# Kernel optimization log

Hardware: AMD Instinct MI355X
Metric: run time of the kernel (lower is better)

## Reference

```python
import jax, jax.numpy as jnp
import numpy as np

D_MODEL = 1024
D_STATE = 16
BATCH = 2
SEQ = 2048


def setup_inputs() -> dict:
    key = jax.random.key(0)
    k1, k2, k3, k4, k5 = jax.random.split(key, 5)
    x = jax.random.normal(k1, (BATCH, SEQ, D_MODEL), dtype=jnp.float32)
    log_A_diag = jax.random.normal(k2, (D_MODEL, D_STATE), dtype=jnp.float32)
    B_w = jax.random.normal(k3, (D_STATE, D_MODEL), dtype=jnp.float32) / np.sqrt(D_MODEL)
    C_w = jax.random.normal(k4, (D_MODEL, D_STATE), dtype=jnp.float32) / np.sqrt(D_STATE)
    D_vec = jax.random.normal(k5, (D_MODEL,), dtype=jnp.float32)
    return {"x": x, "log_A_diag": log_A_diag, "B_w": B_w, "C_w": C_w, "D_vec": D_vec}


def reference(x, log_A_diag, B_w, C_w, D_vec):
    # x: (B, L, D)
    B, L, D = x.shape
    pad = 2 * L
    A_bar = jnp.exp(-jnp.exp(log_A_diag))          # (D, S), in (0, 1)
    B_t = jnp.einsum('bld,sd->bls', x, B_w)        # B projection: (B, L, S)
    k_idx = jnp.arange(L, dtype=x.dtype)
    kernel = A_bar[..., None] ** k_idx             # (D, S, L) exponential kernel
    # zero-padded FFT convolution along time axis
    kernel_fft = jnp.fft.rfft(kernel, n=pad, axis=-1)                 # (D, S, L+1)
    B_fft = jnp.fft.rfft(B_t.transpose(0, 2, 1), n=pad, axis=-1)      # (B, S, L+1)
    conv_fft = kernel_fft[None] * B_fft[:, None]                      # (B, D, S, L+1)
    conv = jnp.fft.irfft(conv_fft, n=pad, axis=-1)[..., :L]           # (B, D, S, L)
    # C projection fused over state dim; equivalent to permute->einsum('blds,ds->bld')
    y = jnp.einsum('bdsl,ds->bld', conv, C_w)
    y = y + D_vec[None, None, :] * x               # skip connection
    return y  # dropout is identity in eval mode
```

## Files before the change

### kernel.cpp

```cpp
#include <hip/hip_runtime.h>

#define D_MODEL 1024
#define D_STATE 16
#define BATCH   2
#define SEQ     2048
#define CHUNK   32
#define NCHUNK  (SEQ / CHUNK)
#define NGRP    (SEQ / 4)

__global__ __launch_bounds__(256) void k_bt(const float* __restrict__ x,
                                            const float* __restrict__ Bw,
                                            float* __restrict__ bt,
                                            float* __restrict__ btg) {
    const int t    = threadIdx.x;
    const int wave = t >> 6;
    const int lane = t & 63;

    float4 bw[4][4];
    const float* bwp = Bw + (wave * 4) * D_MODEL + lane * 16;
#pragma unroll
    for (int i = 0; i < 4; ++i)
#pragma unroll
        for (int k = 0; k < 4; ++k)
            bw[i][k] = *(const float4*)(bwp + i * D_MODEL + k * 4);

    const int ROWS = (BATCH * SEQ) / gridDim.x;
    const int row0 = blockIdx.x * ROWS;
    for (int r = 0; r < ROWS; ++r) {
        const int row = row0 + r;
        const float* xr = x + (size_t)row * D_MODEL + lane * 16;
        float4 xv[4];
#pragma unroll
        for (int k = 0; k < 4; ++k) xv[k] = *(const float4*)(xr + k * 4);

        float acc[4] = {0.f, 0.f, 0.f, 0.f};
#pragma unroll
        for (int i = 0; i < 4; ++i) {
#pragma unroll
            for (int k = 0; k < 4; ++k) {
                acc[i] += xv[k].x * bw[i][k].x;
                acc[i] += xv[k].y * bw[i][k].y;
                acc[i] += xv[k].z * bw[i][k].z;
                acc[i] += xv[k].w * bw[i][k].w;
            }
        }
#pragma unroll
        for (int m = 1; m < 64; m <<= 1) {
#pragma unroll
            for (int i = 0; i < 4; ++i) acc[i] += __shfl_xor(acc[i], m, 64);
        }
        if (lane == 0) {
            *(float4*)(bt + (size_t)row * D_STATE + wave * 4) =
                make_float4(acc[0], acc[1], acc[2], acc[3]);
            const int b = row >> 11;
            const int l = row & (SEQ - 1);
            float* p = btg + (((size_t)(b * NGRP + (l >> 2)) * D_STATE + wave * 4) << 2) + (l & 3);
#pragma unroll
            for (int i = 0; i < 4; ++i) p[i * 4] = acc[i];
        }
    }
}

__global__ __launch_bounds__(128) void k_scan(const float* __restrict__ btg,
                                              const float* __restrict__ logA,
                                              float* __restrict__ carry) {
    const int g = blockIdx.x * 128 + threadIdx.x;
    const int s = g & 15;
    const int d = (g >> 4) & (D_MODEL - 1);
    const int b = g >> 14;

    const float A  = expf(-expf(logA[d * D_STATE + s]));
    const float A2 = A * A;
    const float A4 = A2 * A2;

    const float4* bp = (const float4*)btg + (size_t)b * NGRP * D_STATE + s;
    size_t ci = (size_t)b * NCHUNK * (D_MODEL * D_STATE) + d * D_STATE + s;

    float h = 0.f;
    for (int c = 0; c < NCHUNK; ++c) {
        carry[ci] = h;
        ci += D_MODEL * D_STATE;
#pragma unroll
        for (int gg = 0; gg < CHUNK / 4; ++gg) {
            const float4 v = bp[(size_t)(c * (CHUNK / 4) + gg) * D_STATE];
            h = h * A4 + (((v.x * A + v.y) * A + v.z) * A + v.w);
        }
    }
}

__global__ __launch_bounds__(256) void k_final(const float* __restrict__ x,
                                               const float* __restrict__ logA,
                                               const float* __restrict__ Cw,
                                               const float* __restrict__ Dv,
                                               const float* __restrict__ bt,
                                               const float* __restrict__ carry,
                                               float* __restrict__ y) {
    const int blk = blockIdx.x;
    const int dt  = blk & 3;
    const int c   = (blk >> 2) & (NCHUNK - 1);
    const int b   = blk >> 8;
    const int t   = threadIdx.x;
    const int d   = dt * 256 + t;

    float A[D_STATE], C[D_STATE], h[D_STATE];
    const float* lp = logA + (size_t)d * D_STATE;
    const float* cp = Cw + (size_t)d * D_STATE;
    const float* hp = carry + ((size_t)(b * NCHUNK + c) * D_MODEL + d) * D_STATE;
#pragma unroll
    for (int s = 0; s < D_STATE; ++s) {
        A[s] = expf(-expf(lp[s]));
        C[s] = cp[s];
        h[s] = hp[s];
    }
    const float dv = Dv[d];

    const float* btrow = bt + (size_t)(b * SEQ + c * CHUNK) * D_STATE;
    const size_t rowbase = (size_t)(b * SEQ + c * CHUNK) * D_MODEL + d;
    const float* xp = x + rowbase;
    float*       yp = y + rowbase;

#pragma unroll 4
    for (int j = 0; j < CHUNK; ++j) {
        float acc = dv * xp[(size_t)j * D_MODEL];
#pragma unroll
        for (int s = 0; s < D_STATE; ++s) {
            h[s] = A[s] * h[s] + btrow[j * D_STATE + s];
            acc += C[s] * h[s];
        }
        yp[(size_t)j * D_MODEL] = acc;
    }
}

extern "C" void kernel_launch(void* const* d_in, const int* in_sizes, int n_in,
                              void* d_out, int out_size, void* d_ws, size_t ws_size,
                              hipStream_t stream) {
    const float* x    = (const float*)d_in[0];
    const float* logA = (const float*)d_in[1];
    const float* Bw   = (const float*)d_in[2];
    const float* Cw   = (const float*)d_in[3];
    const float* Dv   = (const float*)d_in[4];
    float* y = (float*)d_out;

    float* bt    = (float*)d_ws;
    float* btg   = bt  + (size_t)BATCH * SEQ * D_STATE;
    float* carry = btg + (size_t)BATCH * SEQ * D_STATE;

    hipLaunchKernelGGL(k_bt,    dim3(512), dim3(256), 0, stream, x, Bw, bt, btg);
    hipLaunchKernelGGL(k_scan,  dim3((BATCH * D_MODEL * D_STATE) / 128), dim3(128), 0, stream, btg, logA, carry);
    hipLaunchKernelGGL(k_final, dim3(BATCH * NCHUNK * (D_MODEL / 256)),  dim3(256), 0, stream, x, logA, Cw, Dv, bt, carry, y);
}
```

Before: 116.8 us.

## Split sequential chunk scan into parallel sub-blocks with shared-memory carry combine

The carry scan now splits the sequence into 8 sub-blocks, each handled by a separate group of threads, instead of one thread walking all 64 chunks. Each group computes local chunk carries from zero, the final sub-block states are combined through shared memory using powers of A, and the corrected carries are written out. This shortens the serial dependency chain in the scan, which had only 32K threads each doing 2048 sequential steps, and raises parallelism. In exchange it adds a shared-memory sync, extra registers for the local carries, and repeated powering of A, which may add some rounding differences.

```diff
diff --git a/kernel.cpp b/kernel.cpp
--- a/kernel.cpp
+++ b/kernel.cpp
@@ -7,6 +7,10 @@
 #define CHUNK   32
 #define NCHUNK  (SEQ / CHUNK)
 #define NGRP    (SEQ / 4)
+#define Q       8
+#define SBLEN   (SEQ / Q)
+#define SBGRP   (SBLEN / 4)
+#define SBCHK   (SBLEN / CHUNK)
 
 __global__ __launch_bounds__(256) void k_bt(const float* __restrict__ x,
                                             const float* __restrict__ Bw,
@@ -61,30 +65,51 @@
     }
 }
 
-__global__ __launch_bounds__(128) void k_scan(const float* __restrict__ btg,
+__global__ __launch_bounds__(256) void k_scan(const float* __restrict__ btg,
                                               const float* __restrict__ logA,
                                               float* __restrict__ carry) {
-    const int g = blockIdx.x * 128 + threadIdx.x;
-    const int s = g & 15;
-    const int d = (g >> 4) & (D_MODEL - 1);
-    const int b = g >> 14;
+    const int blk = blockIdx.x;
+    const int b   = blk >> 9;
+    const int dp  = blk & 511;
+    const int t   = threadIdx.x;
+    const int q   = t >> 5;
+    const int ds  = t & 31;
+    const int s   = ds & 15;
+    const int d   = dp * 2 + (ds >> 4);
 
     const float A  = expf(-expf(logA[d * D_STATE + s]));
-    const float A2 = A * A;
-    const float A4 = A2 * A2;
+    const float A2 = A * A,    A4 = A2 * A2;
+    const float A8 = A4 * A4,  A16 = A8 * A8,  A32 = A16 * A16;
+    const float A64 = A32 * A32, A128 = A64 * A64, A256 = A128 * A128;
 
-    const float4* bp = (const float4*)btg + (size_t)b * NGRP * D_STATE + s;
-    size_t ci = (size_t)b * NCHUNK * (D_MODEL * D_STATE) + d * D_STATE + s;
+    const float4* bp = (const float4*)btg + ((size_t)b * NGRP + q * SBGRP) * D_STATE + s;
 
+    float localC[SBCHK];
     float h = 0.f;
-    for (int c = 0; c < NCHUNK; ++c) {
-        carry[ci] = h;
-        ci += D_MODEL * D_STATE;
+#pragma unroll
+    for (int k = 0; k < SBCHK; ++k) {
+        localC[k] = h;
 #pragma unroll
         for (int gg = 0; gg < CHUNK / 4; ++gg) {
-            const float4 v = bp[(size_t)(c * (CHUNK / 4) + gg) * D_STATE];
+            const float4 v = bp[(size_t)(k * (CHUNK / 4) + gg) * D_STATE];
             h = h * A4 + (((v.x * A + v.y) * A + v.z) * A + v.w);
         }
+    }
+
+    __shared__ float Fs[32][Q + 1];
+    Fs[ds][q] = h;
+    __syncthreads();
+
+    float H = 0.f;
+    for (int p = 0; p < q; ++p) H = H * A256 + Fs[ds][p];
+
+    float fac = H;
+    size_t ci = (((size_t)(b * NCHUNK + q * SBCHK)) * D_MODEL + d) * D_STATE + s;
+#pragma unroll
+    for (int k = 0; k < SBCHK; ++k) {
+        carry[ci] = localC[k] + fac;
+        fac *= A32;
+        ci += (size_t)D_MODEL * D_STATE;
     }
 }
 
@@ -146,6 +171,6 @@
     float* carry = btg + (size_t)BATCH * SEQ * D_STATE;
 
     hipLaunchKernelGGL(k_bt,    dim3(512), dim3(256), 0, stream, x, Bw, bt, btg);
-    hipLaunchKernelGGL(k_scan,  dim3((BATCH * D_MODEL * D_STATE) / 128), dim3(128), 0, stream, btg, logA, carry);
-    hipLaunchKernelGGL(k_final, dim3(BATCH * NCHUNK * (D_MODEL / 256)),  dim3(256), 0, stream, x, logA, Cw, Dv, bt, carry, y);
+    hipLaunchKernelGGL(k_scan,  dim3(BATCH * (D_MODEL / 2)), dim3(256), 0, stream, btg, logA, carry);
+    hipLaunchKernelGGL(k_final, dim3(BATCH * NCHUNK * (D_MODEL / 256)), dim3(256), 0, stream, x, logA, Cw, Dv, bt, carry, y);
 }
```

Measured after the change: 102.5 us. -12.2%, faster.
